# Kernel tuning notes

Hardware: AMD Instinct MI355X
Metric: run time of the kernel (lower is better)

Reference implementation:

```python
import jax, jax.numpy as jnp
import numpy as np

N_NODES = 100000
N_EDGES = 1600000   # avg in-degree 16
D_IN = 128
D_HID = 256
N_CLASSES = 40
N_GRAPHS = 64


def setup_inputs() -> dict:
    key = jax.random.key(0)
    ks = jax.random.split(key, 8)
    h = jax.random.normal(ks[0], (N_NODES, D_IN), dtype=jnp.float32)
    src = jax.random.randint(ks[1], (N_EDGES,), 0, N_NODES, dtype=jnp.int64)
    dst = jax.random.randint(ks[2], (N_EDGES,), 0, N_NODES, dtype=jnp.int64)
    graph_ids = jnp.sort(jax.random.randint(ks[3], (N_NODES,), 0, N_GRAPHS, dtype=jnp.int64))
    s_in = 1.0 / np.sqrt(D_IN)
    s_hid = 1.0 / np.sqrt(D_HID)
    W_self = jax.random.uniform(ks[4], (D_IN, D_HID), jnp.float32, -s_in, s_in)
    W_neigh = jax.random.uniform(ks[5], (D_IN, D_HID), jnp.float32, -s_in, s_in)
    b = jnp.zeros((D_HID,), jnp.float32)
    W_pred = jax.random.uniform(ks[6], (D_HID, N_CLASSES), jnp.float32, -s_hid, s_hid)
    b_pred = jnp.zeros((N_CLASSES,), jnp.float32)
    return {"h": h, "W_self": W_self, "W_neigh": W_neigh, "b": b,
            "W_pred": W_pred, "b_pred": b_pred,
            "src": src, "dst": dst, "graph_ids": graph_ids}


def reference(h, W_self, W_neigh, b, W_pred, b_pred, src, dst, graph_ids):
    n_nodes = h.shape[0]
    # --- SAGEConv 'mean': mean over in-neighbors (gather src feats, scatter-add to dst) ---
    deg = jax.ops.segment_sum(jnp.ones_like(dst, dtype=h.dtype), dst, num_segments=n_nodes)
    agg = jax.ops.segment_sum(h[src], dst, num_segments=n_nodes)  # [N, D_IN]
    h_neigh = agg / jnp.maximum(deg, 1.0)[:, None]  # zero-in-degree -> 0
    hid = jax.nn.relu(h @ W_self + h_neigh @ W_neigh + b)  # [N, D_HID]
    # --- AvgPooling per graph ---
    cnt = jax.ops.segment_sum(jnp.ones((n_nodes,), h.dtype), graph_ids, num_segments=N_GRAPHS)
    pooled = jax.ops.segment_sum(hid, graph_ids, num_segments=N_GRAPHS) / jnp.maximum(cnt, 1.0)[:, None]
    # --- prediction head (dropout is identity in eval) ---
    return pooled @ W_pred + b_pred  # [N_GRAPHS, N_CLASSES]
```

## Files before the change

### kernel.cpp

```cpp
#include <hip/hip_runtime.h>
#include <stdint.h>

constexpr int kNodes    = 100000;
constexpr int kEdges    = 1600000;
constexpr int kDin      = 128;
constexpr int kK        = 256;
constexpr int kDhid     = 256;
constexpr int kClasses  = 40;
constexpr int kGraphs   = 64;

constexpr int kBktShift = 8;
constexpr int NB = (kNodes + 255) >> 8;
constexpr int kBktCap = 5120;
constexpr int kChunk = 6250;
constexpr int kEBlocks = kEdges / kChunk;
constexpr int kSCT = 1024;
constexpr int kCvtBlocks = (kNodes * 32 + kK * kDhid) / kSCT;

constexpr int kTPB = 3;
constexpr int kTiles = kNodes / 32;
constexpr int kGemmBlocks = (kTiles + kTPB - 1) / kTPB;

typedef __attribute__((ext_vector_type(8))) short bf8_t;
typedef __attribute__((ext_vector_type(4))) float f4_t;
typedef __attribute__((ext_vector_type(2))) float f2_t;

__device__ inline ushort f2bf(float f) {
  uint32_t u = __float_as_uint(f);
  u += 0x7fff + ((u >> 16) & 1);
  return (ushort)(u >> 16);
}

template <bool HI>
__device__ inline f2_t fp8x2_f32(uint32_t w) {
#if __has_builtin(__builtin_amdgcn_cvt_pk_f32_fp8)
  return __builtin_amdgcn_cvt_pk_f32_fp8(w, HI);
#else
  f2_t r;
  uint32_t b0 = HI ? ((w >> 16) & 0xffu) : (w & 0xffu);
  uint32_t b1 = HI ? (w >> 24) : ((w >> 8) & 0xffu);
  auto dec = [](uint32_t b) -> float {
    uint32_t s = (b & 0x80u) << 24;
    uint32_t em = b & 0x7fu;
    float mag;
    if (em >= 0x08u) {
      uint32_t e = (em >> 3) - 7 + 127;
      mag = __uint_as_float((e << 23) | ((em & 7u) << 20));
    } else {
      mag = (float)em * 0.001953125f;
    }
    return __uint_as_float(s | __float_as_uint(mag));
  };
  r.x = dec(b0); r.y = dec(b1);
  return r;
#endif
}

__device__ inline uint32_t f32_to_e4m3(float f) {
  uint32_t sgn = (__float_as_uint(f) >> 31) << 7;
  float mag = fabsf(f);
  uint32_t r;
  if (mag >= 0.015625f) {
    uint32_t u = __float_as_uint(mag);
    u += 0x7FFFF + ((u >> 20) & 1);
    int e = (int)(u >> 23) - 127;
    if (e > 8) r = 0x7Eu;
    else r = (uint32_t)((e + 7) << 3) | ((u >> 20) & 7u);
  } else {
    float m = mag * 512.f;
    int mi = (int)rintf(m);
    r = (mi > 7) ? 0x08u : (uint32_t)mi;
  }
  return r | sgn;
}

__device__ inline uint32_t pack4_e4m3(float x, float y, float z, float w) {
#if __has_builtin(__builtin_amdgcn_cvt_pk_fp8_f32)
  uint32_t p = __builtin_amdgcn_cvt_pk_fp8_f32(x, y, 0u, false);
  return __builtin_amdgcn_cvt_pk_fp8_f32(z, w, p, true);
#else
  return f32_to_e4m3(x) | (f32_to_e4m3(y) << 8) |
         (f32_to_e4m3(z) << 16) | (f32_to_e4m3(w) << 24);
#endif
}

__global__ __launch_bounds__(kSCT)
void scatter_cvt(const int* __restrict__ src, const int* __restrict__ dst,
                 int* __restrict__ bktCur, uint32_t* __restrict__ pairs,
                 const float* __restrict__ h, const float* __restrict__ Ws,
                 const float* __restrict__ Wn, ushort* __restrict__ A16,
                 ushort* __restrict__ Wt, uint8_t* __restrict__ H8,
                 int scatterBlocks) {
  __shared__ int hist[NB], base[NB], cur[NB];
  if ((int)blockIdx.x < scatterBlocks) {
    for (int i = threadIdx.x; i < NB; i += kSCT) { hist[i] = 0; cur[i] = 0; }
    __syncthreads();
    int e0 = blockIdx.x * kChunk;
    int e1 = min(e0 + kChunk, kEdges);
    for (int e = e0 + threadIdx.x; e < e1; e += kSCT)
      atomicAdd(&hist[dst[e] >> kBktShift], 1);
    __syncthreads();
    for (int i = threadIdx.x; i < NB; i += kSCT)
      base[i] = hist[i] ? atomicAdd(&bktCur[i], hist[i]) : 0;
    __syncthreads();
    for (int e = e0 + threadIdx.x; e < e1; e += kSCT) {
      int d = dst[e];
      int b = d >> kBktShift;
      int p = atomicAdd(&cur[b], 1);
      pairs[(size_t)b * kBktCap + base[b] + p] = ((uint32_t)src[e] << 8) | (uint32_t)(d & 255);
    }
  } else {
    int t = ((int)blockIdx.x - scatterBlocks) * kSCT + threadIdx.x;
    const int hN = kNodes * 32;
    if (t < hN) {
      int n = t >> 5;
      int c4 = (t & 31) * 4;
      float4 v = *reinterpret_cast<const float4*>(h + (size_t)n * kDin + c4);
      ushort4 o;
      o.x = f2bf(v.x); o.y = f2bf(v.y); o.z = f2bf(v.z); o.w = f2bf(v.w);
      *reinterpret_cast<ushort4*>(A16 + (size_t)n * kK + c4) = o;
      *reinterpret_cast<uint32_t*>(H8 + (size_t)n * kDin + c4) =
          pack4_e4m3(v.x, v.y, v.z, v.w);
    } else {
      int u = t - hN;
      int j = u & 255;
      int k = u >> 8;
      float v = (k < 128) ? Ws[(size_t)k * kDhid + j] : Wn[(size_t)(k - 128) * kDhid + j];
      Wt[(size_t)j * kK + k] = f2bf(v);
    }
  }
}

__global__ void bucket_fill(const uint32_t* __restrict__ pairs, const int* __restrict__ bktCur,
                            int* __restrict__ row, int* __restrict__ rend,
                            int* __restrict__ csr) {
  __shared__ int deg[256], scn[256], cur[256];
  int b = blockIdx.x;
  int t = threadIdx.x;
  int cnt = bktCur[b];
  int e0 = b * kBktCap;
  int nb0 = b << kBktShift;
  deg[t] = 0;
  __syncthreads();
  for (int e = t; e < cnt; e += 256)
    atomicAdd(&deg[pairs[e0 + e] & 255u], 1);
  __syncthreads();
  int d = deg[t];
  scn[t] = d;
  __syncthreads();
#pragma unroll
  for (int off = 1; off < 256; off <<= 1) {
    int u = (t >= off) ? scn[t - off] : 0;
    __syncthreads();
    scn[t] += u;
    __syncthreads();
  }
  int excl = scn[t] - d;
  cur[t] = excl;
  int n = nb0 + t;
  if (n < kNodes) { row[n] = e0 + excl; rend[n] = e0 + scn[t]; }
  __syncthreads();
  for (int e = t; e < cnt; e += 256) {
    uint32_t pr = pairs[e0 + e];
    int p = atomicAdd(&cur[pr & 255u], 1);
    csr[e0 + p] = (int)(pr >> 8);
  }
}

__global__ void aggregate8(const uint8_t* __restrict__ H8, ushort* __restrict__ A16,
                           const int* __restrict__ row, const int* __restrict__ rend,
                           const int* __restrict__ csr) {
  int wv = (blockIdx.x * 256 + threadIdx.x) >> 6;
  int lane = threadIdx.x & 63;
  int grp = lane >> 4;
  int sub = lane & 15;
  int n = wv * 4 + grp;
  int s0 = row[n], s1 = rend[n];
  float a0 = 0.f, a1 = 0.f, a2 = 0.f, a3 = 0.f, a4 = 0.f, a5 = 0.f, a6 = 0.f, a7 = 0.f;
#pragma unroll 4
  for (int i = s0; i < s1; ++i) {
    int s = csr[i];
    uint2 v = *reinterpret_cast<const uint2*>(H8 + (size_t)s * kDin + sub * 8);
    f2_t l0 = fp8x2_f32<false>(v.x), h0 = fp8x2_f32<true>(v.x);
    f2_t l1 = fp8x2_f32<false>(v.y), h1 = fp8x2_f32<true>(v.y);
    a0 += l0.x; a1 += l0.y; a2 += h0.x; a3 += h0.y;
    a4 += l1.x; a5 += l1.y; a6 += h1.x; a7 += h1.y;
  }
  float rd = 1.f / fmaxf((float)(s1 - s0), 1.f);
  uint4 o;
  o.x = (uint32_t)f2bf(a0 * rd) | ((uint32_t)f2bf(a1 * rd) << 16);
  o.y = (uint32_t)f2bf(a2 * rd) | ((uint32_t)f2bf(a3 * rd) << 16);
  o.z = (uint32_t)f2bf(a4 * rd) | ((uint32_t)f2bf(a5 * rd) << 16);
  o.w = (uint32_t)f2bf(a6 * rd) | ((uint32_t)f2bf(a7 * rd) << 16);
  *reinterpret_cast<uint4*>((char*)A16 + (size_t)n * 512 + 256 + sub * 16) = o;
}

__global__ __launch_bounds__(256, 2)
void gemm_pool(const ushort* __restrict__ A16, const ushort* __restrict__ Wt,
               const float* __restrict__ bias, const int* __restrict__ gid,
               float* __restrict__ gsum) {
  __shared__ ushort Abuf[2][32 * 256];
  const int tid  = threadIdx.x;
  const int lane = tid & 63;
  const int wave = tid >> 6;
  const int lhi = lane >> 4;
  const int llo = lane & 15;

  bf8_t bfr[4][8];
#pragma unroll
  for (int nf = 0; nf < 4; ++nf) {
    const char* wrow = (const char*)Wt + (size_t)(wave * 64 + nf * 16 + llo) * 512 + lhi * 16;
#pragma unroll
    for (int kk = 0; kk < 8; ++kk)
      bfr[nf][kk] = *reinterpret_cast<const bf8_t*>(wrow + kk * 64);
  }
  float bv[4];
#pragma unroll
  for (int nf = 0; nf < 4; ++nf) bv[nf] = bias[wave * 64 + nf * 16 + llo];

  auto stage = [&](int buf, int tile) {
#pragma unroll
    for (int i = 0; i < 4; ++i) {
      int r = i * 8 + (tid >> 5);
      int wb = (tid & 31) * 16;
      size_t gsrc = ((size_t)tile * 32 + r) * 512 + (size_t)(wb ^ ((r & 7) << 4));
      uint32_t ldst = (uint32_t)(i * 4096 + tid * 16);
      __builtin_amdgcn_global_load_lds(
          (const __attribute__((address_space(1))) uint32_t*)((const char*)A16 + gsrc),
          (__attribute__((address_space(3))) uint32_t*)((char*)&Abuf[buf][0] + ldst),
          16, 0, 0);
    }
  };

  const int t0 = blockIdx.x * kTPB;
  const int nt = min(kTPB, kTiles - t0);
  stage(0, t0);
  __syncthreads();

  float pooled[4] = {0.f, 0.f, 0.f, 0.f};
  int cur_g = gid[t0 * 32];

  for (int ti = 0; ti < nt; ++ti) {
    int tile = t0 + ti;
    if (ti + 1 < nt) stage((ti + 1) & 1, tile + 1);

    f4_t acc[2][4];
#pragma unroll
    for (int mf = 0; mf < 2; ++mf)
#pragma unroll
      for (int nf = 0; nf < 4; ++nf) acc[mf][nf] = (f4_t)0.f;
    const char* abase = (const char*)&Abuf[ti & 1][0];
    const int swz = (llo & 7) << 4;
#pragma unroll
    for (int kk = 0; kk < 8; ++kk) {
      int kb = kk * 64 + lhi * 16;
      bf8_t x0 = *reinterpret_cast<const bf8_t*>(abase + llo * 512 + (kb ^ swz));
      bf8_t x1 = *reinterpret_cast<const bf8_t*>(abase + (16 + llo) * 512 + (kb ^ swz));
#pragma unroll
      for (int nf = 0; nf < 4; ++nf) {
        acc[0][nf] = __builtin_amdgcn_mfma_f32_16x16x32_bf16(x0, bfr[nf][kk], acc[0][nf], 0, 0, 0);
        acc[1][nf] = __builtin_amdgcn_mfma_f32_16x16x32_bf16(x1, bfr[nf][kk], acc[1][nf], 0, 0, 0);
      }
    }

    int base = tile * 32;
    int gA = gid[base], gB = gid[base + 31];
    if (gA == gB) {
      if (gA != cur_g) {
#pragma unroll
        for (int nf = 0; nf < 4; ++nf) {
          if (pooled[nf] != 0.f)
            atomicAdd(&gsum[cur_g * kDhid + wave * 64 + nf * 16 + llo], pooled[nf]);
          pooled[nf] = 0.f;
        }
        cur_g = gA;
      }
#pragma unroll
      for (int nf = 0; nf < 4; ++nf) {
        float s = 0.f;
#pragma unroll
        for (int mf = 0; mf < 2; ++mf)
#pragma unroll
          for (int q = 0; q < 4; ++q) s += fmaxf(acc[mf][nf][q] + bv[nf], 0.f);
        pooled[nf] += s;
      }
    } else {
#pragma unroll
      for (int mf = 0; mf < 2; ++mf)
#pragma unroll
        for (int q = 0; q < 4; ++q) {
          int r = base + mf * 16 + lhi * 4 + q;
          int g = gid[r];
#pragma unroll
          for (int nf = 0; nf < 4; ++nf) {
            float v = fmaxf(acc[mf][nf][q] + bv[nf], 0.f);
            if (v != 0.f) atomicAdd(&gsum[g * kDhid + wave * 64 + nf * 16 + llo], v);
          }
        }
    }
    __syncthreads();
  }

#pragma unroll
  for (int nf = 0; nf < 4; ++nf)
    if (pooled[nf] != 0.f)
      atomicAdd(&gsum[cur_g * kDhid + wave * 64 + nf * 16 + llo], pooled[nf]);
}

__global__ void head_kernel(const float* __restrict__ gsum,
                            const float* __restrict__ Wp,
                            const float* __restrict__ bp,
                            const int* __restrict__ gid,
                            float* __restrict__ out) {
  int g = blockIdx.x;
  int c = threadIdx.x;
  int lo0 = 0, hi0 = kNodes;
  while (lo0 < hi0) { int m = (lo0 + hi0) >> 1; if (gid[m] < g) lo0 = m + 1; else hi0 = m; }
  int lo1 = lo0, hi1 = kNodes;
  while (lo1 < hi1) { int m = (lo1 + hi1) >> 1; if (gid[m] < g + 1) lo1 = m + 1; else hi1 = m; }
  float rc = 1.0f / fmaxf((float)(lo1 - lo0), 1.0f);
  if (c < kClasses) {
    float acc = bp[c];
    for (int k = 0; k < kDhid; ++k)
      acc += gsum[g * kDhid + k] * rc * Wp[k * kClasses + c];
    out[g * kClasses + c] = acc;
  }
}

extern "C" void kernel_launch(void* const* d_in, const int* in_sizes, int n_in,
                              void* d_out, int out_size, void* d_ws, size_t ws_size,
                              hipStream_t stream) {
  const float* h  = (const float*)d_in[0];
  const float* Ws = (const float*)d_in[1];
  const float* Wn = (const float*)d_in[2];
  const float* b  = (const float*)d_in[3];
  const float* Wp = (const float*)d_in[4];
  const float* bp = (const float*)d_in[5];
  const int* src  = (const int*)d_in[6];
  const int* dst  = (const int*)d_in[7];
  const int* gid  = (const int*)d_in[8];
  float* out = (float*)d_out;

  char* ws = (char*)d_ws;
  const size_t a16Off    = 0;
  const size_t wtOff     = 51249152;
  const size_t csrOff    = 51380224;
  const size_t rowOff    = 59408384;
  const size_t rendOff   = 59808384;
  const size_t gsumOff   = 60208384;
  const size_t bktCurOff = 60273920;
  const size_t h8Off     = 60275712;
  const size_t pairsOff  = 73075712;
  const size_t needBig   = pairsOff + 8028160;
  ushort* A16     = (ushort*)(ws + a16Off);
  ushort* Wt      = (ushort*)(ws + wtOff);
  int* csr        = (int*)(ws + csrOff);
  int* row        = (int*)(ws + rowOff);
  int* rend       = (int*)(ws + rendOff);
  float* gsum     = (float*)(ws + gsumOff);
  int* bktCur     = (int*)(ws + bktCurOff);
  uint8_t* H8     = (uint8_t*)(ws + h8Off);
  const bool bigWs = (ws_size >= needBig);
  uint32_t* pairs = bigWs ? (uint32_t*)(ws + pairsOff) : (uint32_t*)(ws + a16Off);

  (void)hipMemsetAsync(ws + gsumOff, 0, (60273920 + 1568) - 60208384, stream);

  if (bigWs) {
    hipLaunchKernelGGL(scatter_cvt, dim3(kEBlocks + kCvtBlocks), dim3(kSCT), 0, stream,
                       src, dst, bktCur, pairs, h, Ws, Wn, A16, Wt, H8, kEBlocks);
    hipLaunchKernelGGL(bucket_fill, dim3(NB), dim3(256), 0, stream,
                       pairs, bktCur, row, rend, csr);
  } else {
    hipLaunchKernelGGL(scatter_cvt, dim3(kEBlocks), dim3(kSCT), 0, stream,
                       src, dst, bktCur, pairs, h, Ws, Wn, A16, Wt, H8, kEBlocks);
    hipLaunchKernelGGL(bucket_fill, dim3(NB), dim3(256), 0, stream,
                       pairs, bktCur, row, rend, csr);
    hipLaunchKernelGGL(scatter_cvt, dim3(kCvtBlocks), dim3(kSCT), 0, stream,
                       src, dst, bktCur, pairs, h, Ws, Wn, A16, Wt, H8, 0);
  }

  hipLaunchKernelGGL(aggregate8, dim3(kNodes / 16), dim3(256), 0, stream,
                     H8, A16, row, rend, csr);

  hipLaunchKernelGGL(gemm_pool, dim3(kGemmBlocks), dim3(256), 0, stream,
                     A16, Wt, b, gid, gsum);
  hipLaunchKernelGGL(head_kernel, dim3(kGraphs), dim3(64), 0, stream,
                     gsum, Wp, bp, gid, out);
}
```

Measured before the change: 147.3 us.

## Load GEMM A tiles directly from global into registers, dropping LDS staging

```diff
diff --git a/kernel.cpp b/kernel.cpp
--- a/kernel.cpp
+++ b/kernel.cpp
@@ -17,9 +17,9 @@
 constexpr int kSCT = 1024;
 constexpr int kCvtBlocks = (kNodes * 32 + kK * kDhid) / kSCT;
 
-constexpr int kTPB = 3;
+constexpr int kTPB = 5;
 constexpr int kTiles = kNodes / 32;
-constexpr int kGemmBlocks = (kTiles + kTPB - 1) / kTPB;
+constexpr int kGemmBlocks = kTiles / kTPB;
 
 typedef __attribute__((ext_vector_type(8))) short bf8_t;
 typedef __attribute__((ext_vector_type(4))) float f4_t;
@@ -199,7 +199,6 @@
 void gemm_pool(const ushort* __restrict__ A16, const ushort* __restrict__ Wt,
                const float* __restrict__ bias, const int* __restrict__ gid,
                float* __restrict__ gsum) {
-  __shared__ ushort Abuf[2][32 * 256];
   const int tid  = threadIdx.x;
   const int lane = tid & 63;
   const int wave = tid >> 6;
@@ -218,48 +217,33 @@
 #pragma unroll
   for (int nf = 0; nf < 4; ++nf) bv[nf] = bias[wave * 64 + nf * 16 + llo];
 
-  auto stage = [&](int buf, int tile) {
-#pragma unroll
-    for (int i = 0; i < 4; ++i) {
-      int r = i * 8 + (tid >> 5);
-      int wb = (tid & 31) * 16;
-      size_t gsrc = ((size_t)tile * 32 + r) * 512 + (size_t)(wb ^ ((r & 7) << 4));
-      uint32_t ldst = (uint32_t)(i * 4096 + tid * 16);
-      __builtin_amdgcn_global_load_lds(
-          (const __attribute__((address_space(1))) uint32_t*)((const char*)A16 + gsrc),
-          (__attribute__((address_space(3))) uint32_t*)((char*)&Abuf[buf][0] + ldst),
-          16, 0, 0);
-    }
-  };
-
   const int t0 = blockIdx.x * kTPB;
-  const int nt = min(kTPB, kTiles - t0);
-  stage(0, t0);
-  __syncthreads();
-
   float pooled[4] = {0.f, 0.f, 0.f, 0.f};
   int cur_g = gid[t0 * 32];
 
-  for (int ti = 0; ti < nt; ++ti) {
+  for (int ti = 0; ti < kTPB; ++ti) {
     int tile = t0 + ti;
-    if (ti + 1 < nt) stage((ti + 1) & 1, tile + 1);
-
-    f4_t acc[2][4];
-#pragma unroll
-    for (int mf = 0; mf < 2; ++mf)
-#pragma unroll
-      for (int nf = 0; nf < 4; ++nf) acc[mf][nf] = (f4_t)0.f;
-    const char* abase = (const char*)&Abuf[ti & 1][0];
-    const int swz = (llo & 7) << 4;
+    const char* abase = (const char*)A16 + (size_t)tile * 32 * 512;
+
+    bf8_t av0[8], av1[8];
 #pragma unroll
     for (int kk = 0; kk < 8; ++kk) {
       int kb = kk * 64 + lhi * 16;
-      bf8_t x0 = *reinterpret_cast<const bf8_t*>(abase + llo * 512 + (kb ^ swz));
-      bf8_t x1 = *reinterpret_cast<const bf8_t*>(abase + (16 + llo) * 512 + (kb ^ swz));
+      av0[kk] = *reinterpret_cast<const bf8_t*>(abase + llo * 512 + kb);
+      av1[kk] = *reinterpret_cast<const bf8_t*>(abase + (16 + llo) * 512 + kb);
+    }
+
+    f4_t acc[2][4];
+#pragma unroll
+    for (int mf = 0; mf < 2; ++mf)
+#pragma unroll
+      for (int nf = 0; nf < 4; ++nf) acc[mf][nf] = (f4_t)0.f;
+#pragma unroll
+    for (int kk = 0; kk < 8; ++kk) {
 #pragma unroll
       for (int nf = 0; nf < 4; ++nf) {
-        acc[0][nf] = __builtin_amdgcn_mfma_f32_16x16x32_bf16(x0, bfr[nf][kk], acc[0][nf], 0, 0, 0);
-        acc[1][nf] = __builtin_amdgcn_mfma_f32_16x16x32_bf16(x1, bfr[nf][kk], acc[1][nf], 0, 0, 0);
+        acc[0][nf] = __builtin_amdgcn_mfma_f32_16x16x32_bf16(av0[kk], bfr[nf][kk], acc[0][nf], 0, 0, 0);
+        acc[1][nf] = __builtin_amdgcn_mfma_f32_16x16x32_bf16(av1[kk], bfr[nf][kk], acc[1][nf], 0, 0, 0);
       }
     }
 
@@ -298,7 +282,6 @@
           }
         }
     }
-    __syncthreads();
   }
 
 #pragma unroll
```

After: 154.5 us. +4.9%, slower.
